# Kernel tuning notes

Measured on AMD Instinct MI355X. Metric: run time of the kernel, lower is better.

Reference implementation:

```python
import jax, jax.numpy as jnp
import numpy as np

N_NODES = 100000
N_EDGES = 1600000
IN_SIZE = 256
HID = 64
HEADS = 2
OUT_SIZE = 16


def _gat_layer(x, W, a_l, a_r, b, src, dst, n_nodes, heads, feat):
    # x: [N, Din]; W: [Din, H*F]; a_l, a_r: [H, F]; b: [H*F]
    h = (x @ W).reshape(n_nodes, heads, feat)          # [N, H, F]
    el = jnp.sum(h * a_l, axis=-1)                     # [N, H]
    er = jnp.sum(h * a_r, axis=-1)                     # [N, H]
    e = jax.nn.leaky_relu(el[src] + er[dst], 0.2)      # [E, H]
    # segment softmax over incoming edges of each dst node
    m = jax.ops.segment_max(e, dst, num_segments=n_nodes)
    m = jnp.where(jnp.isfinite(m), m, 0.0)             # nodes with no in-edges
    p = jnp.exp(e - m[dst])                            # [E, H]
    s = jax.ops.segment_sum(p, dst, num_segments=n_nodes)
    alpha = p / (s[dst] + 1e-9)                        # [E, H]
    # scatter-add weighted source features
    out = jax.ops.segment_sum(alpha[:, :, None] * h[src], dst, num_segments=n_nodes)
    return out + b.reshape(1, heads, feat)             # [N, H, F]


def setup_inputs() -> dict:
    key = jax.random.key(0)
    ks = jax.random.split(key, 12)
    features = jax.random.normal(ks[0], (N_NODES, IN_SIZE), dtype=jnp.float32)
    src = jax.random.randint(ks[1], (N_EDGES,), 0, N_NODES, dtype=jnp.int32)
    dst = jax.random.randint(ks[2], (N_EDGES,), 0, N_NODES, dtype=jnp.int32)
    s1 = 1.0 / np.sqrt(IN_SIZE)
    s2 = 1.0 / np.sqrt(HID * HEADS)
    W1 = jax.random.normal(ks[3], (IN_SIZE, HEADS * HID), dtype=jnp.float32) * s1
    al1 = jax.random.normal(ks[4], (HEADS, HID), dtype=jnp.float32) * 0.1
    ar1 = jax.random.normal(ks[5], (HEADS, HID), dtype=jnp.float32) * 0.1
    b1 = jnp.zeros((HEADS * HID,), dtype=jnp.float32)
    W2 = jax.random.normal(ks[6], (HEADS * HID, HEADS * HID), dtype=jnp.float32) * s2
    al2 = jax.random.normal(ks[7], (HEADS, HID), dtype=jnp.float32) * 0.1
    ar2 = jax.random.normal(ks[8], (HEADS, HID), dtype=jnp.float32) * 0.1
    b2 = jnp.zeros((HEADS * HID,), dtype=jnp.float32)
    Wl = jax.random.normal(ks[9], (HEADS * HID, OUT_SIZE), dtype=jnp.float32) * s2
    bl = jnp.zeros((OUT_SIZE,), dtype=jnp.float32)
    return {"features": features, "src": src, "dst": dst,
            "W1": W1, "al1": al1, "ar1": ar1, "b1": b1,
            "W2": W2, "al2": al2, "ar2": ar2, "b2": b2,
            "Wl": Wl, "bl": bl}


def reference(features, src, dst, W1, al1, ar1, b1, W2, al2, ar2, b2, Wl, bl):
    n = features.shape[0]
    h = _gat_layer(features, W1, al1, ar1, b1.reshape(HEADS, HID).reshape(-1),
                   src, dst, n, HEADS, HID)
    h = jax.nn.elu(h.reshape(n, HEADS * HID))          # flatten(1) + ELU (dropout: eval)
    h = _gat_layer(h, W2, al2, ar2, b2, src, dst, n, HEADS, HID)
    h = jax.nn.elu(h.reshape(n, HEADS * HID))
    return h @ Wl + bl                                  # [N, OUT_SIZE]
```

## Files before the change

kernel.cpp:

```cpp
#include <hip/hip_runtime.h>
#include <hip/hip_fp16.h>

#define N_NODES 100000
#define N_EDGES 1600000
#define IN_SIZE 256
#define HID 64
#define HEADS 2
#define DMODEL 128
#define OUT_SZ 16

#define BSHIFT 9
#define BNODES 512
#define NB 196
#define CAP 16384
#define EPB 4096

typedef _Float16 f16x4 __attribute__((ext_vector_type(4)));
typedef _Float16 f16x8 __attribute__((ext_vector_type(8)));
typedef float f32x4 __attribute__((ext_vector_type(4)));



__global__ __launch_bounds__(256) void wt_fused_kernel(const float* __restrict__ W1,
                                                       _Float16* __restrict__ Wt1,
                                                       const float* __restrict__ W2,
                                                       _Float16* __restrict__ Wt2,
                                                       int* __restrict__ counts) {
    int tid = threadIdx.x;
    if (blockIdx.x == 0 && tid < NB) counts[tid] = 0;
    int i = blockIdx.x * 256 + tid;
    if (i < 128 * IN_SIZE) {
        int nr = i / IN_SIZE;
        int k = i - nr * IN_SIZE;
        Wt1[i] = (_Float16)W1[(size_t)k * 128 + nr];
    } else {
        int j = i - 128 * IN_SIZE;
        if (j < 128 * DMODEL) {
            int nr = j / DMODEL;
            int k = j - nr * DMODEL;
            Wt2[j] = (_Float16)W2[(size_t)k * 128 + nr];
        }
    }
}


__global__ __launch_bounds__(256) void bin_kernel(const int* __restrict__ src,
                                                  const int* __restrict__ dst,
                                                  int* __restrict__ counts,
                                                  uint32_t* __restrict__ bucketbuf, int e) {
    __shared__ int hist[NB];
    __shared__ int lbase[NB + 1];
    __shared__ int gbase[NB];
    __shared__ uint32_t sbuf[EPB];
    __shared__ int lds[256];
    int tid = threadIdx.x;
    int start = blockIdx.x * EPB;
    for (int i = tid; i < NB; i += 256) hist[i] = 0;
    __syncthreads();
    int pr[16];
    uint32_t pv[16];
    #pragma unroll
    for (int i = 0; i < 16; i++) {
        int idx = start + i * 256 + tid;
        pr[i] = -1;
        if (idx < e) {
            int d = dst[idx];
            int s = src[idx];
            int b = d >> BSHIFT;
            int r = atomicAdd(&hist[b], 1);
            pr[i] = (b << 16) | r;
            pv[i] = ((uint32_t)(d & (BNODES - 1)) << 17) | (uint32_t)s;
        }
    }
    __syncthreads();
    int h = (tid < NB) ? hist[tid] : 0;
    lds[tid] = h;
    __syncthreads();
    for (int off = 1; off < 256; off <<= 1) {
        int x = 0;
        if (tid >= off) x = lds[tid - off];
        __syncthreads();
        lds[tid] += x;
        __syncthreads();
    }
    if (tid < NB) lbase[tid] = lds[tid] - h;
    if (tid == NB - 1) lbase[NB] = lds[tid];
    if (tid < NB) gbase[tid] = atomicAdd(&counts[tid], h);
    __syncthreads();
    #pragma unroll
    for (int i = 0; i < 16; i++) {
        int p = pr[i];
        if (p >= 0) sbuf[lbase[p >> 16] + (p & 0xffff)] = pv[i];
    }
    __syncthreads();
    int total = lbase[NB];
    for (int i = tid; i < total; i += 256) {
        int lo = 0, hi = NB - 1;
        while (lo < hi) {
            int mid = (lo + hi + 1) >> 1;
            if (lbase[mid] <= i) lo = mid; else hi = mid - 1;
        }
        int posg = gbase[lo] + (i - lbase[lo]);
        if (posg < CAP)
            bucketbuf[(size_t)lo * CAP + posg] = sbuf[i];
    }
}


__global__ __launch_bounds__(256) void csr_kernel(const uint32_t* __restrict__ bucketbuf,
                                                  const int* __restrict__ counts,
                                                  int* __restrict__ deg,
                                                  int* __restrict__ offs,
                                                  int* __restrict__ ssrc, int n) {
    __shared__ int hist[BNODES];
    __shared__ int cursor[BNODES];
    __shared__ int lds[256];
    int b = blockIdx.x;
    int tid = threadIdx.x;

    int t = (tid < NB) ? min(counts[tid], CAP) : 0;
    lds[tid] = t;
    __syncthreads();
    for (int off = 1; off < 256; off <<= 1) {
        int x = 0;
        if (tid >= off) x = lds[tid - off];
        __syncthreads();
        lds[tid] += x;
        __syncthreads();
    }
    int base = (b == 0) ? 0 : lds[b - 1];
    int cnt = min(counts[b], CAP);
    __syncthreads();

    int node0 = b << BSHIFT;
    const uint32_t* ebuf = bucketbuf + (size_t)b * CAP;

    hist[tid] = 0;
    hist[tid + 256] = 0;
    __syncthreads();
    for (int i = tid; i < cnt; i += 256)
        atomicAdd(&hist[ebuf[i] >> 17], 1);
    __syncthreads();

    int h0 = hist[2 * tid], h1 = hist[2 * tid + 1];
    lds[tid] = h0 + h1;
    __syncthreads();
    for (int off = 1; off < 256; off <<= 1) {
        int x = 0;
        if (tid >= off) x = lds[tid - off];
        __syncthreads();
        lds[tid] += x;
        __syncthreads();
    }
    int excl = lds[tid] - (h0 + h1);
    cursor[2 * tid] = excl;
    cursor[2 * tid + 1] = excl + h0;
    int g0 = node0 + 2 * tid, g1 = g0 + 1;
    if (g0 < n) { deg[g0] = h0; offs[g0] = base + excl; }
    if (g1 < n) { deg[g1] = h1; offs[g1] = base + excl + h0; }
    __syncthreads();

    for (int i = tid; i < cnt; i += 256) {
        uint32_t ed = ebuf[i];
        int p = atomicAdd(&cursor[ed >> 17], 1);
        ssrc[base + p] = (int)(ed & 0x1FFFF);
    }
}


template <int K, bool F16IN>
__global__ __launch_bounds__(256) void gemm_attn_kernel(const void* __restrict__ Ap,
                                                        const _Float16* __restrict__ Wt,
                                                        const float* __restrict__ al,
                                                        const float* __restrict__ ar,
                                                        uint32_t* __restrict__ h16,
                                                        float* __restrict__ el,
                                                        float* __restrict__ er, int n) {
    __shared__ _Float16 As[64 * 72];
    __shared__ _Float16 Bs[128 * 72];
    int tid = threadIdx.x;
    int w = tid >> 6;
    int lane = tid & 63;
    int c = lane & 15;
    int quad = lane >> 4;
    int r0 = blockIdx.x * 64;

    f32x4 acc[8];
    #pragma unroll
    for (int t = 0; t < 8; t++) acc[t] = (f32x4){0.f, 0.f, 0.f, 0.f};

    for (int kt = 0; kt < K; kt += 64) {
        {
            int lr = tid >> 4;
            int lc = (tid & 15) * 4;
            #pragma unroll
            for (int q = 0; q < 4; q++) {
                int row = lr + 16 * q;
                int gr = r0 + row;
                if constexpr (F16IN) {
                    const uint32_t* Af = (const uint32_t*)Ap;
                    uint2 v = make_uint2(0u, 0u);
                    if (gr < n) v = *(const uint2*)(Af + (size_t)gr * (K / 2) + (kt + lc) / 2);
                    *(uint2*)(As + row * 72 + lc) = v;
                } else {
                    const float* Af = (const float*)Ap;
                    float4 v = make_float4(0.f, 0.f, 0.f, 0.f);
                    if (gr < n) v = *(const float4*)(Af + (size_t)gr * K + kt + lc);
                    f16x4 hv = {(_Float16)v.x, (_Float16)v.y, (_Float16)v.z, (_Float16)v.w};
                    *(f16x4*)(As + row * 72 + lc) = hv;
                }
            }
            int nr = tid >> 1;
            int kc = (tid & 1) * 32;
            const uint4* gsrc = (const uint4*)(Wt + (size_t)nr * K + kt + kc);
            uint4 v0 = gsrc[0];
            uint4 v1 = gsrc[1];
            uint4 v2 = gsrc[2];
            uint4 v3 = gsrc[3];
            *(uint4*)(Bs + nr * 72 + kc + 0)  = v0;
            *(uint4*)(Bs + nr * 72 + kc + 8)  = v1;
            *(uint4*)(Bs + nr * 72 + kc + 16) = v2;
            *(uint4*)(Bs + nr * 72 + kc + 24) = v3;
        }
        __syncthreads();

        #pragma unroll
        for (int kk = 0; kk < 64; kk += 32) {
            f16x8 a = *(const f16x8*)(As + (16 * w + c) * 72 + kk + quad * 8);
            #pragma unroll
            for (int t = 0; t < 8; t++) {
                f16x8 b = *(const f16x8*)(Bs + (16 * t + c) * 72 + kk + quad * 8);
                acc[t] = __builtin_amdgcn_mfma_f32_16x16x32_f16(a, b, acc[t], 0, 0, 0);
            }
        }
        __syncthreads();
    }

    #pragma unroll
    for (int i = 0; i < 4; i++) {
        int gr = r0 + 16 * w + quad * 4 + i;
        float el0 = 0.f, el1 = 0.f, er0 = 0.f, er1 = 0.f;
        #pragma unroll
        for (int t = 0; t < 8; t++) {
            float hv = acc[t][i];
            float alv = al[16 * t + c];
            float arv = ar[16 * t + c];
            if (t < 4) { el0 += hv * alv; er0 += hv * arv; }
            else       { el1 += hv * alv; er1 += hv * arv; }
        }
        #pragma unroll
        for (int off = 1; off < 16; off <<= 1) {
            el0 += __shfl_xor(el0, off);
            el1 += __shfl_xor(el1, off);
            er0 += __shfl_xor(er0, off);
            er1 += __shfl_xor(er1, off);
        }
        if (c == 0 && gr < n) {
            *(float2*)(el + 2 * gr) = make_float2(el0, el1);
            *(float2*)(er + 2 * gr) = make_float2(er0, er1);
        }
        #pragma unroll
        for (int t = 0; t < 8; t++) {
            float own = acc[t][i];
            float other = __shfl_xor(own, 1);
            if ((c & 1) == 0 && gr < n) {
                __half2 hh = __floats2half2_rn(own, other);
                h16[(size_t)gr * 64 + 8 * t + (c >> 1)] = *(const uint32_t*)&hh;
            }
        }
    }
}


__device__ __forceinline__ float edge_w(float2 e, float erh, int head) {
    float x = (head ? e.y : e.x) + erh;
    x = x >= 0.f ? x : 0.2f * x;
    return __expf(x);
}

__device__ __forceinline__ void acc8(uint4 u, float w, float* a) {
    union { uint4 u4; f16x8 h8; } cv;
    cv.u4 = u;
    #pragma unroll
    for (int i = 0; i < 8; i++)
        a[i] = fmaf((float)cv.h8[i], w, a[i]);
}

__global__ __launch_bounds__(256) void agg_kernel(const uint32_t* __restrict__ hb,
                                                  const int* __restrict__ ssrc,
                                                  const float* __restrict__ el,
                                                  const float* __restrict__ er,
                                                  const float* __restrict__ bias,
                                                  const int* __restrict__ offs,
                                                  const int* __restrict__ deg,
                                                  uint32_t* __restrict__ out16, int n) {
    int wid = (blockIdx.x * blockDim.x + threadIdx.x) >> 6;
    int lane = threadIdx.x & 63;
    if (wid >= n) return;
    int start = offs[wid];
    int d = deg[wid];
    int g = lane >> 4;
    int fl = lane & 15;
    int head = fl >> 3;

    float2 erv = *(const float2*)(er + 2 * wid);
    float erh = head ? erv.y : erv.x;

    const int* sp = ssrc + start;
    const float2* el2 = (const float2*)el;
    const char* hbb = (const char*)hb;
    uint32_t foff = (uint32_t)(fl << 4);

    float a[8];
    #pragma unroll
    for (int i = 0; i < 8; i++) a[i] = 0.f;
    float psum = 0.f;

    int j = 0;
    if (d >= 16) {
        int s0 = sp[g];
        int s1 = sp[4 + g];
        int s2 = sp[8 + g];
        int s3 = sp[12 + g];
        for (; j + 32 <= d; j += 16) {
            float2 e0 = el2[s0];
            uint4 u0 = *(const uint4*)(hbb + (((uint32_t)s0 << 8) + foff));
            float2 e1 = el2[s1];
            uint4 u1 = *(const uint4*)(hbb + (((uint32_t)s1 << 8) + foff));
            float2 e2 = el2[s2];
            uint4 u2 = *(const uint4*)(hbb + (((uint32_t)s2 << 8) + foff));
            float2 e3 = el2[s3];
            uint4 u3 = *(const uint4*)(hbb + (((uint32_t)s3 << 8) + foff));
            int ns0 = sp[j + 16 + g];
            int ns1 = sp[j + 20 + g];
            int ns2 = sp[j + 24 + g];
            int ns3 = sp[j + 28 + g];
            float w0 = edge_w(e0, erh, head);
            float w1 = edge_w(e1, erh, head);
            float w2 = edge_w(e2, erh, head);
            float w3 = edge_w(e3, erh, head);
            psum += (w0 + w1) + (w2 + w3);
            acc8(u0, w0, a);
            acc8(u1, w1, a);
            acc8(u2, w2, a);
            acc8(u3, w3, a);
            s0 = ns0; s1 = ns1; s2 = ns2; s3 = ns3;
        }
        {
            float2 e0 = el2[s0];
            uint4 u0 = *(const uint4*)(hbb + (((uint32_t)s0 << 8) + foff));
            float2 e1 = el2[s1];
            uint4 u1 = *(const uint4*)(hbb + (((uint32_t)s1 << 8) + foff));
            float2 e2 = el2[s2];
            uint4 u2 = *(const uint4*)(hbb + (((uint32_t)s2 << 8) + foff));
            float2 e3 = el2[s3];
            uint4 u3 = *(const uint4*)(hbb + (((uint32_t)s3 << 8) + foff));
            float w0 = edge_w(e0, erh, head);
            float w1 = edge_w(e1, erh, head);
            float w2 = edge_w(e2, erh, head);
            float w3 = edge_w(e3, erh, head);
            psum += (w0 + w1) + (w2 + w3);
            acc8(u0, w0, a);
            acc8(u1, w1, a);
            acc8(u2, w2, a);
            acc8(u3, w3, a);
            j += 16;
        }
    }
    for (; j < d; j += 4) {
        int last = d - 1;
        int i0 = j + g;
        int s0 = sp[min(i0, last)];
        float2 e0 = el2[s0];
        uint4 u0 = *(const uint4*)(hbb + (((uint32_t)s0 << 8) + foff));
        float w0 = (i0 <= last) ? edge_w(e0, erh, head) : 0.f;
        psum += w0;
        acc8(u0, w0, a);
    }

    #pragma unroll
    for (int i = 0; i < 8; i++) {
        a[i] += __shfl_xor(a[i], 16);
        a[i] += __shfl_xor(a[i], 32);
    }
    psum += __shfl_xor(psum, 16);
    psum += __shfl_xor(psum, 32);

    if (lane < 16) {
        float inv = 1.f / (psum + 1e-9f);
        float4 b0 = *(const float4*)(bias + 8 * lane);
        float4 b1 = *(const float4*)(bias + 8 * lane + 4);
        float o[8];
        o[0] = fmaf(a[0], inv, b0.x);
        o[1] = fmaf(a[1], inv, b0.y);
        o[2] = fmaf(a[2], inv, b0.z);
        o[3] = fmaf(a[3], inv, b0.w);
        o[4] = fmaf(a[4], inv, b1.x);
        o[5] = fmaf(a[5], inv, b1.y);
        o[6] = fmaf(a[6], inv, b1.z);
        o[7] = fmaf(a[7], inv, b1.w);
        #pragma unroll
        for (int i = 0; i < 8; i++)
            o[i] = o[i] > 0.f ? o[i] : (__expf(o[i]) - 1.f);
        __half2 h01 = __floats2half2_rn(o[0], o[1]);
        __half2 h23 = __floats2half2_rn(o[2], o[3]);
        __half2 h45 = __floats2half2_rn(o[4], o[5]);
        __half2 h67 = __floats2half2_rn(o[6], o[7]);
        uint4 ov = make_uint4(*(const uint32_t*)&h01, *(const uint32_t*)&h23,
                              *(const uint32_t*)&h45, *(const uint32_t*)&h67);
        ((uint4*)(out16 + (size_t)wid * 64))[lane] = ov;
    }
}


__global__ __launch_bounds__(256) void final_kernel(const uint32_t* __restrict__ x16,
                                                    const float* __restrict__ Wl,
                                                    const float* __restrict__ bl,
                                                    float* __restrict__ out, int n) {
    __shared__ float Ws[DMODEL * OUT_SZ];
    __shared__ float bs[OUT_SZ];
    int tid = threadIdx.x;
    for (int i = tid; i < DMODEL * OUT_SZ / 4; i += 256)
        ((float4*)Ws)[i] = ((const float4*)Wl)[i];
    if (tid < OUT_SZ) bs[tid] = bl[tid];
    __syncthreads();
    int node = blockIdx.x * 16 + (tid >> 4);
    int c = tid & 15;
    if (node >= n) return;
    const uint4* xr = (const uint4*)(x16 + (size_t)node * 64);
    float acc = bs[c];
    #pragma unroll
    for (int kk = 0; kk < 16; kk++) {
        uint4 v = xr[kk];
        float2 f0 = __half22float2(*(const __half2*)&v.x);
        float2 f1 = __half22float2(*(const __half2*)&v.y);
        float2 f2 = __half22float2(*(const __half2*)&v.z);
        float2 f3 = __half22float2(*(const __half2*)&v.w);
        acc += f0.x * Ws[(8 * kk + 0) * OUT_SZ + c];
        acc += f0.y * Ws[(8 * kk + 1) * OUT_SZ + c];
        acc += f1.x * Ws[(8 * kk + 2) * OUT_SZ + c];
        acc += f1.y * Ws[(8 * kk + 3) * OUT_SZ + c];
        acc += f2.x * Ws[(8 * kk + 4) * OUT_SZ + c];
        acc += f2.y * Ws[(8 * kk + 5) * OUT_SZ + c];
        acc += f3.x * Ws[(8 * kk + 6) * OUT_SZ + c];
        acc += f3.y * Ws[(8 * kk + 7) * OUT_SZ + c];
    }
    out[(size_t)node * OUT_SZ + c] = acc;
}


extern "C" void kernel_launch(void* const* d_in, const int* in_sizes, int n_in,
                              void* d_out, int out_size, void* d_ws, size_t ws_size,
                              hipStream_t stream) {
    const float* features = (const float*)d_in[0];
    const int*   src      = (const int*)d_in[1];
    const int*   dst      = (const int*)d_in[2];
    const float* W1  = (const float*)d_in[3];
    const float* al1 = (const float*)d_in[4];
    const float* ar1 = (const float*)d_in[5];
    const float* b1  = (const float*)d_in[6];
    const float* W2  = (const float*)d_in[7];
    const float* al2 = (const float*)d_in[8];
    const float* ar2 = (const float*)d_in[9];
    const float* b2  = (const float*)d_in[10];
    const float* Wl  = (const float*)d_in[11];
    const float* bl  = (const float*)d_in[12];
    float* out = (float*)d_out;

    const int n = N_NODES, e = N_EDGES;

    char* w = (char*)d_ws;
    uint32_t* h16 = (uint32_t*)w;       w += (size_t)n * 64 * 4;
    uint32_t* x1  = (uint32_t*)w;       w += (size_t)n * 64 * 4;
    uint32_t* x2  = (uint32_t*)w;       w += 26 * 1024 * 1024;
    float* el   = (float*)w;            w += (size_t)n * 2 * 4;
    float* er   = (float*)w;            w += (size_t)n * 2 * 4;
    int* deg    = (int*)w;              w += 400128;
    int* offs   = (int*)w;              w += 400128;
    int* ssrc   = (int*)w;              w += (size_t)e * 4;
    int* counts = (int*)w;              w += 1024;
    _Float16* Wt1 = (_Float16*)w;       w += 128 * IN_SIZE * 2;
    _Float16* Wt2 = (_Float16*)w;       w += 128 * DMODEL * 2;
    uint32_t* bucketbuf = (uint32_t*)x2;

    const int binBlocks = (e + EPB - 1) / EPB;
    const int wtBlocks = (128 * IN_SIZE + 128 * DMODEL + 255) / 256;
    const int gemmBlocks = (n + 63) / 64;
    const int aggBlocks = (n + 3) / 4;
    const int finalBlocks = (n + 15) / 16;

    wt_fused_kernel<<<wtBlocks, 256, 0, stream>>>(W1, Wt1, W2, Wt2, counts);

    bin_kernel<<<binBlocks, 256, 0, stream>>>(src, dst, counts, bucketbuf, e);
    csr_kernel<<<NB, 256, 0, stream>>>(bucketbuf, counts, deg, offs, ssrc, n);

    gemm_attn_kernel<IN_SIZE, false><<<gemmBlocks, 256, 0, stream>>>(features, Wt1, al1, ar1,
                                                                     h16, el, er, n);
    agg_kernel<<<aggBlocks, 256, 0, stream>>>(h16, ssrc, el, er, b1, offs, deg, x1, n);

    gemm_attn_kernel<DMODEL, true><<<gemmBlocks, 256, 0, stream>>>(x1, Wt2, al2, ar2,
                                                                   h16, el, er, n);
    agg_kernel<<<aggBlocks, 256, 0, stream>>>(h16, ssrc, el, er, b2, offs, deg, x2, n);

    final_kernel<<<finalBlocks, 256, 0, stream>>>(x2, Wl, bl, out, n);

    (void)in_sizes; (void)n_in; (void)out_size; (void)ws_size;
}
```

Before: 427.3 us.

## Merge CSR build with first GEMM in one launch and unroll agg tail

The CSR construction blocks and the first-layer GEMM+attention blocks now run as one kernel launch, split by block index. Since they are independent, they can overlap on the GPU and one launch is removed. The tail loop in the aggregation kernel is also replaced by a single 4-way unrolled pass, so all tail loads are issued together. The cost is a shared LDS buffer sized for the GEMM, which the CSR blocks must also allocate, plus some redundant masked loads in the tail.

```diff
diff --git a/kernel.cpp b/kernel.cpp
--- a/kernel.cpp
+++ b/kernel.cpp
@@ -19,6 +19,8 @@
 typedef _Float16 f16x8 __attribute__((ext_vector_type(8)));
 typedef float f32x4 __attribute__((ext_vector_type(4)));
 
+
+#define GEMM_SMEM (64 * 72 * 2 + 128 * 72 * 2)
 
 
 __global__ __launch_bounds__(256) void wt_fused_kernel(const float* __restrict__ W1,
@@ -107,15 +109,15 @@
 }
 
 
-__global__ __launch_bounds__(256) void csr_kernel(const uint32_t* __restrict__ bucketbuf,
-                                                  const int* __restrict__ counts,
-                                                  int* __restrict__ deg,
-                                                  int* __restrict__ offs,
-                                                  int* __restrict__ ssrc, int n) {
-    __shared__ int hist[BNODES];
-    __shared__ int cursor[BNODES];
-    __shared__ int lds[256];
-    int b = blockIdx.x;
+__device__ __forceinline__ void csr_body(char* smem, int b,
+                                         const uint32_t* __restrict__ bucketbuf,
+                                         const int* __restrict__ counts,
+                                         int* __restrict__ deg,
+                                         int* __restrict__ offs,
+                                         int* __restrict__ ssrc, int n) {
+    int* hist = (int*)smem;
+    int* cursor = hist + BNODES;
+    int* lds = cursor + BNODES;
     int tid = threadIdx.x;
 
     int t = (tid < NB) ? min(counts[tid], CAP) : 0;
@@ -169,21 +171,22 @@
 
 
 template <int K, bool F16IN>
-__global__ __launch_bounds__(256) void gemm_attn_kernel(const void* __restrict__ Ap,
-                                                        const _Float16* __restrict__ Wt,
-                                                        const float* __restrict__ al,
-                                                        const float* __restrict__ ar,
-                                                        uint32_t* __restrict__ h16,
-                                                        float* __restrict__ el,
-                                                        float* __restrict__ er, int n) {
-    __shared__ _Float16 As[64 * 72];
-    __shared__ _Float16 Bs[128 * 72];
+__device__ __forceinline__ void gemm_attn_body(char* smem, int bx,
+                                               const void* __restrict__ Ap,
+                                               const _Float16* __restrict__ Wt,
+                                               const float* __restrict__ al,
+                                               const float* __restrict__ ar,
+                                               uint32_t* __restrict__ h16,
+                                               float* __restrict__ el,
+                                               float* __restrict__ er, int n) {
+    _Float16* As = (_Float16*)smem;
+    _Float16* Bs = (_Float16*)(smem + 64 * 72 * 2);
     int tid = threadIdx.x;
     int w = tid >> 6;
     int lane = tid & 63;
     int c = lane & 15;
     int quad = lane >> 4;
-    int r0 = blockIdx.x * 64;
+    int r0 = bx * 64;
 
     f32x4 acc[8];
     #pragma unroll
@@ -272,6 +275,38 @@
 }
 
 
+__global__ __launch_bounds__(256) void csr_gemm1_kernel(const uint32_t* __restrict__ bucketbuf,
+                                                        const int* __restrict__ counts,
+                                                        int* __restrict__ deg,
+                                                        int* __restrict__ offs,
+                                                        int* __restrict__ ssrc,
+                                                        const float* __restrict__ features,
+                                                        const _Float16* __restrict__ Wt1,
+                                                        const float* __restrict__ al,
+                                                        const float* __restrict__ ar,
+                                                        uint32_t* __restrict__ h16,
+                                                        float* __restrict__ el,
+                                                        float* __restrict__ er, int n) {
+    __shared__ __align__(16) char smem[GEMM_SMEM];
+    if (blockIdx.x < NB)
+        csr_body(smem, blockIdx.x, bucketbuf, counts, deg, offs, ssrc, n);
+    else
+        gemm_attn_body<IN_SIZE, false>(smem, blockIdx.x - NB, features, Wt1,
+                                       al, ar, h16, el, er, n);
+}
+
+__global__ __launch_bounds__(256) void gemm_attn2_kernel(const void* __restrict__ Ap,
+                                                         const _Float16* __restrict__ Wt,
+                                                         const float* __restrict__ al,
+                                                         const float* __restrict__ ar,
+                                                         uint32_t* __restrict__ h16,
+                                                         float* __restrict__ el,
+                                                         float* __restrict__ er, int n) {
+    __shared__ __align__(16) char smem[GEMM_SMEM];
+    gemm_attn_body<DMODEL, true>(smem, blockIdx.x, Ap, Wt, al, ar, h16, el, er, n);
+}
+
+
 __device__ __forceinline__ float edge_w(float2 e, float erh, int head) {
     float x = (head ? e.y : e.x) + erh;
     x = x >= 0.f ? x : 0.2f * x;
@@ -367,15 +402,30 @@
             j += 16;
         }
     }
-    for (; j < d; j += 4) {
+    if (j < d) {
         int last = d - 1;
-        int i0 = j + g;
+        int i0 = j + g, i1 = j + 4 + g, i2 = j + 8 + g, i3 = j + 12 + g;
         int s0 = sp[min(i0, last)];
+        int s1 = sp[min(i1, last)];
+        int s2 = sp[min(i2, last)];
+        int s3 = sp[min(i3, last)];
         float2 e0 = el2[s0];
         uint4 u0 = *(const uint4*)(hbb + (((uint32_t)s0 << 8) + foff));
+        float2 e1 = el2[s1];
+        uint4 u1 = *(const uint4*)(hbb + (((uint32_t)s1 << 8) + foff));
+        float2 e2 = el2[s2];
+        uint4 u2 = *(const uint4*)(hbb + (((uint32_t)s2 << 8) + foff));
+        float2 e3 = el2[s3];
+        uint4 u3 = *(const uint4*)(hbb + (((uint32_t)s3 << 8) + foff));
         float w0 = (i0 <= last) ? edge_w(e0, erh, head) : 0.f;
-        psum += w0;
+        float w1 = (i1 <= last) ? edge_w(e1, erh, head) : 0.f;
+        float w2 = (i2 <= last) ? edge_w(e2, erh, head) : 0.f;
+        float w3 = (i3 <= last) ? edge_w(e3, erh, head) : 0.f;
+        psum += (w0 + w1) + (w2 + w3);
         acc8(u0, w0, a);
+        acc8(u1, w1, a);
+        acc8(u2, w2, a);
+        acc8(u3, w3, a);
     }
 
     #pragma unroll
@@ -492,14 +542,13 @@
     wt_fused_kernel<<<wtBlocks, 256, 0, stream>>>(W1, Wt1, W2, Wt2, counts);
 
     bin_kernel<<<binBlocks, 256, 0, stream>>>(src, dst, counts, bucketbuf, e);
-    csr_kernel<<<NB, 256, 0, stream>>>(bucketbuf, counts, deg, offs, ssrc, n);
-
-    gemm_attn_kernel<IN_SIZE, false><<<gemmBlocks, 256, 0, stream>>>(features, Wt1, al1, ar1,
-                                                                     h16, el, er, n);
+    csr_gemm1_kernel<<<NB + gemmBlocks, 256, 0, stream>>>(bucketbuf, counts, deg, offs, ssrc,
+                                                          features, Wt1, al1, ar1,
+                                                          h16, el, er, n);
+
     agg_kernel<<<aggBlocks, 256, 0, stream>>>(h16, ssrc, el, er, b1, offs, deg, x1, n);
 
-    gemm_attn_kernel<DMODEL, true><<<gemmBlocks, 256, 0, stream>>>(x1, Wt2, al2, ar2,
-                                                                   h16, el, er, n);
+    gemm_attn2_kernel<<<gemmBlocks, 256, 0, stream>>>(x1, Wt2, al2, ar2, h16, el, er, n);
     agg_kernel<<<aggBlocks, 256, 0, stream>>>(h16, ssrc, el, er, b2, offs, deg, x2, n);
 
     final_kernel<<<finalBlocks, 256, 0, stream>>>(x2, Wl, bl, out, n);
```

Result: faster. 399.4 us (-6.5%).
